# Kernel optimization log

Measured on AMD Instinct MI355X. Metric: run time of the kernel, lower is better.

The kernel has to match this reference:

```python
import jax, jax.numpy as jnp
import numpy as np

MAX_THRESHOLD = 0.95


def leaky_clamp(x, lo, hi, slope):
    # identity inside [lo, hi], linear with `slope` outside
    return jnp.where(x < lo, lo + slope * (x - lo),
                     jnp.where(x > hi, hi + slope * (x - hi), x))


def or_gate_layer(x, W, tau_adder):
    # x: (B, in), W: (out, in)
    in_f = W.shape[1]
    tau_floor = float(np.log(in_f - 1) + np.log(MAX_THRESHOLD) - np.log(1.0 - MAX_THRESHOLD))
    tau = tau_floor + jax.nn.leaky_relu(tau_adder, negative_slope=0.05)
    aw = leaky_clamp(W, 0.0, 1.0, 0.1)           # (out, in)
    z = x[:, None, :] * aw[None, :, :]           # (B, out, in) broadcast
    p = jax.nn.softmax(tau * z, axis=-1)         # tau-scaled softmax over in
    return jnp.sum(p * z, axis=-1)               # (B, out)


def setup_inputs() -> dict:
    key = jax.random.key(0)
    ks = jax.random.split(key, 9)
    input_dim = 512
    layer_dims = [1024, 512, 256, 128]
    x = jax.random.uniform(ks[0], (128, input_dim), dtype=jnp.float32)
    in_dim = input_dim * 2
    out = {"x": x}
    for i, out_dim in enumerate(layer_dims):
        out[f"W{i}"] = jax.random.normal(ks[1 + i], (out_dim, in_dim), dtype=jnp.float32)
        out[f"tau{i}"] = jnp.zeros((), dtype=jnp.float32)
        in_dim = out_dim  # only_inverter=True
    return out


def reference(x, W0, W1, W2, W3, tau0, tau1, tau2, tau3):
    h = jnp.concatenate([x, 1.0 - x], axis=-1)   # pass_invert
    for W, t in ((W0, tau0), (W1, tau1), (W2, tau2), (W3, tau3)):
        h = 1.0 - or_gate_layer(h, W, t)         # only_inverter: invert after every layer
    return h
```

## Files before the change

### kernel.cpp

```cpp
#include <hip/hip_runtime.h>
#include <math.h>

#if defined(__has_builtin)
#  if __has_builtin(__builtin_amdgcn_exp2f)
#    define EXP2F(x) __builtin_amdgcn_exp2f(x)
#  endif
#endif
#ifndef EXP2F
#  define EXP2F(x) __expf(0.69314718055994530942f * (x))
#endif

template <int IN, int OUT, bool FIRST>
__launch_bounds__(256)
__global__ void or_layer(const float* __restrict__ hin,
                         const float* __restrict__ W,
                         const float* __restrict__ tau_ptr,
                         float* __restrict__ hout,
                         float tau_floor) {
  constexpr int BB = 4;
  constexpr int OB = 4;
  constexpr int NIT = IN / 256;
  constexpr int nOT = OUT / OB;

  const int lane = threadIdx.x & 63;
  const int wid  = threadIdx.x >> 6;
  const int ot = blockIdx.x % nOT;
  const int bs = blockIdx.x / nOT;
  const int b0 = (bs * 4 + wid) * BB;
  const int o0 = ot * OB;

  const float ta  = tau_ptr[0];
  const float tau = tau_floor + (ta >= 0.0f ? ta : 0.05f * ta);
  const float c2  = tau * 1.44269504088896340736f;

  const float4* __restrict__ Wv = (const float4*)W;
  const float4* __restrict__ Hv = (const float4*)hin;

  float s[BB][OB], t[BB][OB];
#pragma unroll
  for (int r = 0; r < BB; ++r)
#pragma unroll
    for (int c = 0; c < OB; ++c) { s[r][c] = 0.0f; t[r][c] = 0.0f; }

#pragma unroll 2
  for (int ic = 0; ic < NIT; ++ic) {
    const int i4 = ic * 64 + lane;

    float hc[BB][4];
    if (FIRST) {
      constexpr int HALF4 = IN / 8;
      if (i4 < HALF4) {
#pragma unroll
        for (int r = 0; r < BB; ++r) {
          float4 v = Hv[(b0 + r) * HALF4 + i4];
          hc[r][0] = v.x; hc[r][1] = v.y; hc[r][2] = v.z; hc[r][3] = v.w;
        }
      } else {
#pragma unroll
        for (int r = 0; r < BB; ++r) {
          float4 v = Hv[(b0 + r) * HALF4 + (i4 - HALF4)];
          hc[r][0] = 1.0f - v.x; hc[r][1] = 1.0f - v.y;
          hc[r][2] = 1.0f - v.z; hc[r][3] = 1.0f - v.w;
        }
      }
    } else {
#pragma unroll
      for (int r = 0; r < BB; ++r) {
        float4 v = Hv[(b0 + r) * (IN / 4) + i4];
        hc[r][0] = v.x; hc[r][1] = v.y; hc[r][2] = v.z; hc[r][3] = v.w;
      }
    }

    float cw[OB][4];
#pragma unroll
    for (int c = 0; c < OB; ++c) {
      float4 v = Wv[(o0 + c) * (IN / 4) + i4];
      float wj[4] = {v.x, v.y, v.z, v.w};
#pragma unroll
      for (int j = 0; j < 4; ++j) {
        const float m  = fminf(fmaxf(wj[j], 0.0f), 1.0f);
        const float aw = fmaf(0.1f, wj[j] - m, m);
        cw[c][j] = c2 * aw;
      }
    }

#pragma unroll
    for (int r = 0; r < BB; ++r)
#pragma unroll
      for (int c = 0; c < OB; ++c)
#pragma unroll
        for (int j = 0; j < 4; ++j) {
          const float arg = cw[c][j] * hc[r][j];
          const float e   = EXP2F(arg);
          s[r][c] += e;
          t[r][c]  = fmaf(arg, e, t[r][c]);
        }
  }

#pragma unroll
  for (int m = 1; m < 64; m <<= 1) {
#pragma unroll
    for (int r = 0; r < BB; ++r)
#pragma unroll
      for (int c = 0; c < OB; ++c) {
        s[r][c] += __shfl_xor(s[r][c], m, 64);
        t[r][c] += __shfl_xor(t[r][c], m, 64);
      }
  }

  if (lane == 0) {
    const float inv_c2 = 1.0f / c2;
#pragma unroll
    for (int r = 0; r < BB; ++r)
#pragma unroll
      for (int c = 0; c < OB; ++c) {
        const float out = t[r][c] / s[r][c] * inv_c2;
        hout[(b0 + r) * OUT + (o0 + c)] = 1.0f - out;
      }
  }
}

extern "C" void kernel_launch(void* const* d_in, const int* in_sizes, int n_in,
                              void* d_out, int out_size, void* d_ws, size_t ws_size,
                              hipStream_t stream) {
  const float* x    = (const float*)d_in[0];
  const float* W0   = (const float*)d_in[1];
  const float* tau0 = (const float*)d_in[2];
  const float* W1   = (const float*)d_in[3];
  const float* tau1 = (const float*)d_in[4];
  const float* W2   = (const float*)d_in[5];
  const float* tau2 = (const float*)d_in[6];
  const float* W3   = (const float*)d_in[7];
  const float* tau3 = (const float*)d_in[8];

  float* h1  = (float*)d_ws;
  float* h2  = h1 + 128 * 1024;
  float* h3  = h2 + 128 * 512;
  float* out = (float*)d_out;

  const double LOGR = 2.9444389791664403;
  const float tf1024 = (float)(log(1023.0) + LOGR);
  const float tf512  = (float)(log(511.0)  + LOGR);
  const float tf256  = (float)(log(255.0)  + LOGR);

  or_layer<1024, 1024, true ><<<2048, 256, 0, stream>>>(x,  W0, tau0, h1,  tf1024);
  or_layer<1024,  512, false><<<1024, 256, 0, stream>>>(h1, W1, tau1, h2,  tf1024);
  or_layer< 512,  256, false><<< 512, 256, 0, stream>>>(h2, W2, tau2, h3,  tf512);
  or_layer< 256,  128, false><<< 256, 256, 0, stream>>>(h3, W3, tau3, out, tf256);
}
```

Baseline: 130.8 us.

## Split wavefront into 16-lane groups with per-layer batch tiling

Each 64-lane wavefront now handles 8 outputs as four 16-lane groups (2 outputs each) instead of one group reducing 4 outputs across all 64 lanes. The batch tile per block becomes a per-layer template parameter (8, 8, 4, 2), and all four waves in a block share the same batch rows. This shortens the cross-lane shuffle reduction and changes grid sizes and data reuse: W is reused across more batch rows and hidden rows across waves. The trade-offs are fewer blocks in the early layers, more registers for BB=8, and less coalesced 16-lane W loads.

Result: faster. 124.7 us (-4.7%).

```diff
diff --git a/kernel.cpp b/kernel.cpp
--- a/kernel.cpp
+++ b/kernel.cpp
@@ -10,24 +10,26 @@
 #  define EXP2F(x) __expf(0.69314718055994530942f * (x))
 #endif
 
-template <int IN, int OUT, bool FIRST>
+template <int IN, int OUT, int BB, bool FIRST>
 __launch_bounds__(256)
 __global__ void or_layer(const float* __restrict__ hin,
                          const float* __restrict__ W,
                          const float* __restrict__ tau_ptr,
                          float* __restrict__ hout,
                          float tau_floor) {
-  constexpr int BB = 4;
-  constexpr int OB = 4;
-  constexpr int NIT = IN / 256;
-  constexpr int nOT = OUT / OB;
+  constexpr int OBB = 2;
+  constexpr int NIT = IN / 64;
+  constexpr int nOT = OUT / 32;
 
   const int lane = threadIdx.x & 63;
   const int wid  = threadIdx.x >> 6;
+  const int il   = lane & 15;
+  const int og   = lane >> 4;
+
   const int ot = blockIdx.x % nOT;
-  const int bs = blockIdx.x / nOT;
-  const int b0 = (bs * 4 + wid) * BB;
-  const int o0 = ot * OB;
+  const int bt = blockIdx.x / nOT;
+  const int b0 = bt * BB;
+  const int o0 = ot * 32 + wid * 8 + og * OBB;
 
   const float ta  = tau_ptr[0];
   const float tau = tau_floor + (ta >= 0.0f ? ta : 0.05f * ta);
@@ -36,15 +38,15 @@
   const float4* __restrict__ Wv = (const float4*)W;
   const float4* __restrict__ Hv = (const float4*)hin;
 
-  float s[BB][OB], t[BB][OB];
+  float s[BB][OBB], t[BB][OBB];
 #pragma unroll
   for (int r = 0; r < BB; ++r)
 #pragma unroll
-    for (int c = 0; c < OB; ++c) { s[r][c] = 0.0f; t[r][c] = 0.0f; }
+    for (int c = 0; c < OBB; ++c) { s[r][c] = 0.0f; t[r][c] = 0.0f; }
 
 #pragma unroll 2
   for (int ic = 0; ic < NIT; ++ic) {
-    const int i4 = ic * 64 + lane;
+    const int i4 = ic * 16 + il;
 
     float hc[BB][4];
     if (FIRST) {
@@ -71,9 +73,9 @@
       }
     }
 
-    float cw[OB][4];
+    float cw[OBB][4];
 #pragma unroll
-    for (int c = 0; c < OB; ++c) {
+    for (int c = 0; c < OBB; ++c) {
       float4 v = Wv[(o0 + c) * (IN / 4) + i4];
       float wj[4] = {v.x, v.y, v.z, v.w};
 #pragma unroll
@@ -87,7 +89,7 @@
 #pragma unroll
     for (int r = 0; r < BB; ++r)
 #pragma unroll
-      for (int c = 0; c < OB; ++c)
+      for (int c = 0; c < OBB; ++c)
 #pragma unroll
         for (int j = 0; j < 4; ++j) {
           const float arg = cw[c][j] * hc[r][j];
@@ -98,22 +100,22 @@
   }
 
 #pragma unroll
-  for (int m = 1; m < 64; m <<= 1) {
+  for (int m = 1; m < 16; m <<= 1) {
 #pragma unroll
     for (int r = 0; r < BB; ++r)
 #pragma unroll
-      for (int c = 0; c < OB; ++c) {
+      for (int c = 0; c < OBB; ++c) {
         s[r][c] += __shfl_xor(s[r][c], m, 64);
         t[r][c] += __shfl_xor(t[r][c], m, 64);
       }
   }
 
-  if (lane == 0) {
+  if (il == 0) {
     const float inv_c2 = 1.0f / c2;
 #pragma unroll
     for (int r = 0; r < BB; ++r)
 #pragma unroll
-      for (int c = 0; c < OB; ++c) {
+      for (int c = 0; c < OBB; ++c) {
         const float out = t[r][c] / s[r][c] * inv_c2;
         hout[(b0 + r) * OUT + (o0 + c)] = 1.0f - out;
       }
@@ -143,8 +145,8 @@
   const float tf512  = (float)(log(511.0)  + LOGR);
   const float tf256  = (float)(log(255.0)  + LOGR);
 
-  or_layer<1024, 1024, true ><<<2048, 256, 0, stream>>>(x,  W0, tau0, h1,  tf1024);
-  or_layer<1024,  512, false><<<1024, 256, 0, stream>>>(h1, W1, tau1, h2,  tf1024);
-  or_layer< 512,  256, false><<< 512, 256, 0, stream>>>(h2, W2, tau2, h3,  tf512);
-  or_layer< 256,  128, false><<< 256, 256, 0, stream>>>(h3, W3, tau3, out, tf256);
+  or_layer<1024, 1024, 8, true ><<<32 * 16, 256, 0, stream>>>(x,  W0, tau0, h1,  tf1024);
+  or_layer<1024,  512, 8, false><<<16 * 16, 256, 0, stream>>>(h1, W1, tau1, h2,  tf1024);
+  or_layer< 512,  256, 4, false><<< 8 * 32, 256, 0, stream>>>(h2, W2, tau2, h3,  tf512);
+  or_layer< 256,  128, 2, false><<< 4 * 64, 256, 0, stream>>>(h3, W3, tau3, out, tf256);
 }
```
